# Kernel optimization log

Hardware: AMD Instinct MI355X
Metric: run time of the kernel (lower is better)

The kernel has to match this reference:

```python
import jax, jax.numpy as jnp
import numpy as np
from jax import lax

SD = 16          # sample_duration
STRIDE = 16      # feat_stride
SCALES = (4, 8, 16)
RATIOS = (0.5, 1.0, 2.0)
PRE_NMS = 1000   # proposals kept before NMS (TEST config)
POST_NMS = 128   # proposals kept after NMS
NMS_TH = 0.7


def _anchors2d():
    base = 16.0
    ctr = (base - 1.0) / 2.0
    out = []
    for r in RATIOS:
        ws = np.round(np.sqrt(base * base / r))
        hs = np.round(ws * r)
        for s in SCALES:
            w, h = ws * s, hs * s
            out.append([ctr - (w - 1) / 2, ctr - (h - 1) / 2,
                        ctr + (w - 1) / 2, ctr + (h - 1) / 2])
    return np.asarray(out, np.float32)                       # (9, 4)


def _anchors3d():
    # tube anchors: (x1, y1, t1, x2, y2, t2), durations [SD, SD/2, SD/4]
    a2 = _anchors2d()
    out = []
    for d in (SD, SD // 2, SD // 4):
        for a in a2:
            out.append([a[0], a[1], 0.0, a[2], a[3], d - 1.0])
    return np.asarray(out, np.float32)                       # (27, 6)


def _shifted(anchors, H, W):
    k = anchors.shape[-1]
    sx = jnp.arange(W, dtype=jnp.float32) * STRIDE
    sy = jnp.arange(H, dtype=jnp.float32) * STRIDE
    if k == 4:
        sh = jnp.stack(jnp.broadcast_arrays(sx[None, :], sy[:, None],
                                            sx[None, :], sy[:, None]), -1)
    else:
        z = jnp.zeros((H, W), jnp.float32)
        sh = jnp.stack(jnp.broadcast_arrays(sx[None, :], sy[:, None], z,
                                            sx[None, :], sy[:, None], z), -1)
    return (sh[:, :, None, :] + jnp.asarray(anchors)[None, None]).reshape(-1, k)


def _decode(anchors, deltas):
    # deltas layout: (d_ctr..., d_logsize...); works for 2D (k=4) and 3D (k=6)
    nd = anchors.shape[-1] // 2
    lo, hi = anchors[..., :nd], anchors[..., nd:]
    size = hi - lo + 1.0
    ctr = lo + 0.5 * (size - 1.0)
    pctr = deltas[..., :nd] * size + ctr
    psize = jnp.exp(deltas[..., nd:]) * size
    return jnp.concatenate([pctr - 0.5 * (psize - 1.0),
                            pctr + 0.5 * (psize - 1.0)], -1)


def _iou(b, boxes):
    # b: (k,), boxes: (N, k); area/volume IoU with +1 pixel convention
    nd = boxes.shape[-1] // 2
    lo = jnp.maximum(b[:nd], boxes[:, :nd])
    hi = jnp.minimum(b[nd:], boxes[:, nd:])
    inter = jnp.prod(jnp.maximum(hi - lo + 1.0, 0.0), -1)
    va = jnp.prod(b[nd:] - b[:nd] + 1.0)
    vb = jnp.prod(boxes[:, nd:] - boxes[:, :nd] + 1.0, -1)
    return inter / (va + vb - inter)


def _nms(boxes):
    # boxes already sorted by descending score; greedy NMS, fixed output size
    N = boxes.shape[0]

    def body(i, c):
        supp, keep = c
        idx = jnp.argmax(~supp)                 # first unsuppressed box
        keep = keep.at[i].set(idx.astype(jnp.int32))
        supp = supp | (_iou(boxes[idx], boxes) > NMS_TH)
        supp = supp.at[idx].set(True)
        return supp, keep

    _, keep = lax.fori_loop(0, POST_NMS, body,
                            (jnp.zeros(N, bool), jnp.zeros(POST_NMS, jnp.int32)))
    return keep


def _proposals(scores, deltas, anchors, maxs):
    # scores (B,N), deltas (B,N,k), anchors (N,k), maxs (B,1,k)
    boxes = jnp.clip(_decode(anchors[None], deltas), 0.0, maxs)
    _, idx = lax.top_k(scores, PRE_NMS)
    bx = jnp.take_along_axis(boxes, idx[..., None], axis=1)   # (B,PRE,k)
    keep = jax.vmap(_nms)(bx)                                 # (B,POST)
    sel = jnp.take_along_axis(bx, keep[..., None], axis=1)    # (B,POST,k)
    bidx = jnp.broadcast_to(
        jnp.arange(sel.shape[0], dtype=sel.dtype)[:, None, None],
        sel.shape[:2] + (1,))
    return lax.stop_gradient(jnp.concatenate([bidx, sel], -1))


def setup_inputs() -> dict:
    k = jax.random.split(jax.random.key(0), 8)
    s = 0.01
    return {
        "base_feat": jax.random.normal(k[0], (1, 256, 16, 32, 32), jnp.float32),
        "im_info": jnp.array([[512.0, 512.0, 1.0]], jnp.float32),
        "gt_boxes": jax.random.uniform(k[1], (1, 5, 7), jnp.float32) * 100.0,
        "gt_rois": jax.random.uniform(k[2], (1, 5, 16, 5), jnp.float32) * 100.0,
        "W_conv": jax.random.normal(k[3], (512, 256, 3, 3, 3), jnp.float32) * s,
        "b_conv": jnp.zeros((512,), jnp.float32),
        "W_cls": jax.random.normal(k[4], (54, 512), jnp.float32) * s,
        "b_cls": jnp.zeros((54,), jnp.float32),
        "W_bbox": jax.random.normal(k[5], (162, 512), jnp.float32) * s,
        "b_bbox": jnp.zeros((162,), jnp.float32),
        "W_cls16": jax.random.normal(k[6], (18, 512), jnp.float32) * s,
        "b_cls16": jnp.zeros((18,), jnp.float32),
        "W_bbox16": jax.random.normal(k[7], (36, 512), jnp.float32) * s,
        "b_bbox16": jnp.zeros((36,), jnp.float32),
    }


def reference(base_feat, im_info, gt_boxes, gt_rois, W_conv, b_conv,
              W_cls, b_cls, W_bbox, b_bbox, W_cls16, b_cls16,
              W_bbox16, b_bbox16):
    B, _, T, H, W = base_feat.shape
    # RPN_Conv: 3x3x3 Conv3d + ReLU
    conv1 = jax.nn.relu(
        lax.conv_general_dilated(base_feat, W_conv, (1, 1, 1), "SAME",
                                 dimension_numbers=("NCDHW", "OIDHW", "NCDHW"))
        + b_conv[None, :, None, None, None])
    # 1x1x1 score / bbox heads (3D)
    cls3 = jnp.einsum("bcthw,oc->bothw", conv1, W_cls) + b_cls[None, :, None, None, None]
    bbox3 = jnp.einsum("bcthw,oc->bothw", conv1, W_bbox) + b_bbox[None, :, None, None, None]
    # permute(0,1,3,4,2).mean(4) == mean over the temporal axis
    feat2 = conv1.mean(axis=2)
    cls2 = jnp.einsum("bchw,oc->bohw", feat2, W_cls16) + b_cls16[None, :, None, None]
    bbox2 = jnp.einsum("bchw,oc->bohw", feat2, W_bbox16) + b_bbox16[None, :, None, None]
    # reshape(x,2) + softmax over dim 1; fg prob is the second half of channels
    fg3 = jax.nn.softmax(cls3.reshape(B, 2, 27, T, H, W), axis=1)[:, 1]  # (B,27,T,H,W)
    fg2 = jax.nn.softmax(cls2.reshape(B, 2, 9, H, W), axis=1)[:, 1]      # (B,9,H,W)
    # proposal layers consume detached tensors (torch .data)
    fg3, fg2, bbox3d, bbox2d = map(lax.stop_gradient, (fg3, fg2, bbox3, bbox2))
    # flatten position-major (h, w, anchor)
    sc3 = fg3.mean(axis=2).transpose(0, 2, 3, 1).reshape(B, -1)
    dl3 = bbox3d.mean(axis=2).reshape(B, 27, 6, H, W).transpose(0, 3, 4, 1, 2).reshape(B, -1, 6)
    sc2 = fg2.transpose(0, 2, 3, 1).reshape(B, -1)
    dl2 = bbox2d.reshape(B, 9, 4, H, W).transpose(0, 3, 4, 1, 2).reshape(B, -1, 4)
    imh, imw = im_info[:, 0][:, None], im_info[:, 1][:, None]
    sdm = jnp.full_like(imw, SD - 1.0)
    max3 = jnp.stack([imw - 1, imh - 1, sdm, imw - 1, imh - 1, sdm], -1)  # (B,1,6)
    max2 = jnp.stack([imw - 1, imh - 1, imw - 1, imh - 1], -1)            # (B,1,4)
    rois = _proposals(sc3, dl3, _shifted(_anchors3d(), H, W), max3)       # (B,POST,7)
    rois16 = _proposals(sc2, dl2, _shifted(_anchors2d(), H, W), max2)     # (B,POST,5)
    z = jnp.zeros((), jnp.float32)  # eval mode: all RPN losses are 0
    return rois, rois16, z, z, z, z
```

## Files before the change

### kernel.cpp

```cpp
#include <hip/hip_runtime.h>
#include <hip/hip_bf16.h>
#include <cfloat>
#include <cstdint>


#define T_DIM 16
#define H_DIM 32
#define W_DIM 32
#define NVOX  (T_DIM*H_DIM*W_DIM)
#define HW    (H_DIM*W_DIM)
#define CIN   256
#define COUT  512
#define PRE_NMS 1000
#define POST_NMS 128
#define NMS_TH 0.7f

typedef __attribute__((ext_vector_type(8))) short v8s;
typedef __attribute__((ext_vector_type(4))) float v4f;
typedef __attribute__((ext_vector_type(4))) int v4i;

#define MFMA_B16(A,B,C) __builtin_amdgcn_mfma_f32_16x16x32_bf16(A,B,C,0,0,0)

__device__ __forceinline__ short f2bf(float x) {
    unsigned u = __float_as_uint(x);
    u += 0x7FFFu + ((u >> 16) & 1u);
    return (short)(u >> 16);
}
__device__ __forceinline__ float bf2f(short s) {
    return __uint_as_float(((unsigned)(unsigned short)s) << 16);
}
__device__ __forceinline__ int pk(short a, short b) {
    return (int)((unsigned short)a | ((unsigned)(unsigned short)b << 16));
}

__constant__ float c_ws[3] = {23.f, 16.f, 11.f};
__constant__ float c_hs[3] = {12.f, 16.f, 22.f};
__constant__ float c_sc[3] = {4.f, 8.f, 16.f};
__constant__ float c_depth[3] = {16.f, 8.f, 4.f};

__global__ void k_split_w(const float* __restrict__ W, short* __restrict__ A0,
                          short* __restrict__ A1, short* __restrict__ A2) {
    int i = blockIdx.x * 256 + threadIdx.x;
    int c = i & 255;
    int o = (i >> 8) & 511;
    int tap = i >> 17;
    float x = W[(o * 256 + c) * 27 + tap];
    short h = f2bf(x); float r = x - bf2f(h);
    short m = f2bf(r); float r2 = r - bf2f(m);
    short l = f2bf(r2);
    A0[i] = h; A1[i] = m; A2[i] = l;
}

__global__ void k_build_wcomb(const float* __restrict__ Wcls, const float* __restrict__ Wbb,
                              float* __restrict__ Wc) {
    int i = blockIdx.x * 256 + threadIdx.x;
    int o = i & 255;
    int c = i >> 8;
    float v = 0.f;
    if (o < 54) v = Wcls[o * 512 + c];
    else if (o < 216) v = Wbb[(o - 54) * 512 + c];
    Wc[i] = v;
}


#define SP8(X0,X1,X2,X3,X4,X5,X6,X7, OH, OM, OL) {                            \
    short h0_=f2bf(X0), h1_=f2bf(X1), h2_=f2bf(X2), h3_=f2bf(X3);             \
    short h4_=f2bf(X4), h5_=f2bf(X5), h6_=f2bf(X6), h7_=f2bf(X7);             \
    float r0_=(X0)-bf2f(h0_), r1_=(X1)-bf2f(h1_), r2_=(X2)-bf2f(h2_);         \
    float r3_=(X3)-bf2f(h3_), r4_=(X4)-bf2f(h4_), r5_=(X5)-bf2f(h5_);         \
    float r6_=(X6)-bf2f(h6_), r7_=(X7)-bf2f(h7_);                             \
    short m0_=f2bf(r0_), m1_=f2bf(r1_), m2_=f2bf(r2_), m3_=f2bf(r3_);         \
    short m4_=f2bf(r4_), m5_=f2bf(r5_), m6_=f2bf(r6_), m7_=f2bf(r7_);         \
    short l0_=f2bf(r0_-bf2f(m0_)), l1_=f2bf(r1_-bf2f(m1_));                   \
    short l2_=f2bf(r2_-bf2f(m2_)), l3_=f2bf(r3_-bf2f(m3_));                   \
    short l4_=f2bf(r4_-bf2f(m4_)), l5_=f2bf(r5_-bf2f(m5_));                   \
    short l6_=f2bf(r6_-bf2f(m6_)), l7_=f2bf(r7_-bf2f(m7_));                   \
    OH = (v4i){pk(h0_,h1_), pk(h2_,h3_), pk(h4_,h5_), pk(h6_,h7_)};           \
    OM = (v4i){pk(m0_,m1_), pk(m2_,m3_), pk(m4_,m5_), pk(m6_,m7_)};           \
    OL = (v4i){pk(l0_,l1_), pk(l2_,l3_), pk(l4_,l5_), pk(l6_,l7_)};           \
}

#define CV_SHIFT(TAP) {                                                       \
    int kt_ = (TAP) / 9 - 1, kh_ = ((TAP) / 3) % 3 - 1, kw_ = (TAP) % 3 - 1;  \
    int tt_ = bt + kt_, hh_ = bh + kh_, ww_ = bw + kw_;                       \
    bVal = ((unsigned)tt_ < 16u) && ((unsigned)hh_ < 32u) && ((unsigned)ww_ < 32u); \
    bOff = (tt_ << 10) + (hh_ << 5) + ww_;                                    \
}

#define CV_LOAD_A(TAP, CK) {                                                  \
    size_t ao_ = ((size_t)((TAP) * 512 + o0 + sa_o) << 8) + (CK) + sa_kh * 16;\
    qa00 = *(const v4i*)(A0 + ao_); qa01 = *(const v4i*)(A0 + ao_ + 8);       \
    qa10 = *(const v4i*)(A1 + ao_); qa11 = *(const v4i*)(A1 + ao_ + 8);       \
    qa20 = *(const v4i*)(A2 + ao_); qa21 = *(const v4i*)(A2 + ao_ + 8);       \
}

#define CV_LOAD_B(CK) {                                                       \
    const float* ip_ = I + ((size_t)((CK) + sa_kh * 16) << 14) + bOff;        \
    float x0_  = bVal ? ip_[0]        : 0.f;                                  \
    float x1_  = bVal ? ip_[1 << 14]  : 0.f;                                  \
    float x2_  = bVal ? ip_[2 << 14]  : 0.f;                                  \
    float x3_  = bVal ? ip_[3 << 14]  : 0.f;                                  \
    float x4_  = bVal ? ip_[4 << 14]  : 0.f;                                  \
    float x5_  = bVal ? ip_[5 << 14]  : 0.f;                                  \
    float x6_  = bVal ? ip_[6 << 14]  : 0.f;                                  \
    float x7_  = bVal ? ip_[7 << 14]  : 0.f;                                  \
    float x8_  = bVal ? ip_[8 << 14]  : 0.f;                                  \
    float x9_  = bVal ? ip_[9 << 14]  : 0.f;                                  \
    float x10_ = bVal ? ip_[10 << 14] : 0.f;                                  \
    float x11_ = bVal ? ip_[11 << 14] : 0.f;                                  \
    float x12_ = bVal ? ip_[12 << 14] : 0.f;                                  \
    float x13_ = bVal ? ip_[13 << 14] : 0.f;                                  \
    float x14_ = bVal ? ip_[14 << 14] : 0.f;                                  \
    float x15_ = bVal ? ip_[15 << 14] : 0.f;                                  \
    SP8(x0_,x1_,x2_,x3_,x4_,x5_,x6_,x7_,   pbh0, pbm0, pbl0);                 \
    SP8(x8_,x9_,x10_,x11_,x12_,x13_,x14_,x15_, pbh1, pbm1, pbl1);             \
}

__global__ __launch_bounds__(256) void k_conv3d_mfma(
        const float* __restrict__ I, const short* __restrict__ A0,
        const short* __restrict__ A1, const short* __restrict__ A2,
        const float* __restrict__ bias, float* __restrict__ O) {
    __shared__ __align__(16) short Ash[3][4][128][8];
    __shared__ __align__(16) short Bsh[3][4][128][8];
    const int tid = threadIdx.x;
    const int o0 = blockIdx.y * 128;
    const int v0 = blockIdx.x * 128;
    const int lane = tid & 63, wv = tid >> 6;
    const int quad = lane >> 4, m16 = lane & 15;

    const int sa_o = tid >> 1, sa_kh = tid & 1;
    const int vbase = v0 + sa_o;
    const int bt = vbase >> 10, bh = (vbase >> 5) & 31, bw = vbase & 31;

    v4f acc[2][8];
#pragma unroll
    for (int i = 0; i < 2; i++)
#pragma unroll
        for (int j = 0; j < 8; j++) acc[i][j] = (v4f){0.f, 0.f, 0.f, 0.f};

    int bOff, bVal;
    v4i qa00, qa01, qa10, qa11, qa20, qa21;
    v4i pbh0, pbh1, pbm0, pbm1, pbl0, pbl1;

    CV_SHIFT(0);
    CV_LOAD_A(0, 0);
    CV_LOAD_B(0);

    const int ar0 = wv * 32 + m16;
    const int ar1 = ar0 + 16;

    for (int s = 0; s < 216; ++s) {
        __syncthreads();
        *(v4i*)(&Ash[0][sa_kh * 2    ][sa_o][0]) = qa00;
        *(v4i*)(&Ash[0][sa_kh * 2 + 1][sa_o][0]) = qa01;
        *(v4i*)(&Ash[1][sa_kh * 2    ][sa_o][0]) = qa10;
        *(v4i*)(&Ash[1][sa_kh * 2 + 1][sa_o][0]) = qa11;
        *(v4i*)(&Ash[2][sa_kh * 2    ][sa_o][0]) = qa20;
        *(v4i*)(&Ash[2][sa_kh * 2 + 1][sa_o][0]) = qa21;
        *(v4i*)(&Bsh[0][sa_kh * 2    ][sa_o][0]) = pbh0;
        *(v4i*)(&Bsh[0][sa_kh * 2 + 1][sa_o][0]) = pbh1;
        *(v4i*)(&Bsh[1][sa_kh * 2    ][sa_o][0]) = pbm0;
        *(v4i*)(&Bsh[1][sa_kh * 2 + 1][sa_o][0]) = pbm1;
        *(v4i*)(&Bsh[2][sa_kh * 2    ][sa_o][0]) = pbl0;
        *(v4i*)(&Bsh[2][sa_kh * 2 + 1][sa_o][0]) = pbl1;
        __syncthreads();
        {
            int s1 = s + 1;
            if (s1 < 216) {
                int tap1 = s1 >> 3, ck1 = (s1 & 7) << 5;
                if ((s1 & 7) == 0) CV_SHIFT(tap1);
                CV_LOAD_A(tap1, ck1);
                CV_LOAD_B(ck1);
            }
        }
        v8s ah0 = *(const v8s*)(&Ash[0][quad][ar0][0]);
        v8s ah1 = *(const v8s*)(&Ash[0][quad][ar1][0]);
        v8s am0 = *(const v8s*)(&Ash[1][quad][ar0][0]);
        v8s am1 = *(const v8s*)(&Ash[1][quad][ar1][0]);
        v8s al0 = *(const v8s*)(&Ash[2][quad][ar0][0]);
        v8s al1 = *(const v8s*)(&Ash[2][quad][ar1][0]);
#pragma unroll
        for (int vt = 0; vt < 8; ++vt) {
            int vr = vt * 16 + m16;
            v8s bb = *(const v8s*)(&Bsh[0][quad][vr][0]);
            v8s bm = *(const v8s*)(&Bsh[1][quad][vr][0]);
            v8s bl = *(const v8s*)(&Bsh[2][quad][vr][0]);
            v4f a0 = acc[0][vt];
            a0 = MFMA_B16(ah0, bb, a0);
            a0 = MFMA_B16(ah0, bm, a0);
            a0 = MFMA_B16(am0, bb, a0);
            a0 = MFMA_B16(ah0, bl, a0);
            a0 = MFMA_B16(am0, bm, a0);
            a0 = MFMA_B16(al0, bb, a0);
            acc[0][vt] = a0;
            v4f a1 = acc[1][vt];
            a1 = MFMA_B16(ah1, bb, a1);
            a1 = MFMA_B16(ah1, bm, a1);
            a1 = MFMA_B16(am1, bb, a1);
            a1 = MFMA_B16(ah1, bl, a1);
            a1 = MFMA_B16(am1, bm, a1);
            a1 = MFMA_B16(al1, bb, a1);
            acc[1][vt] = a1;
        }
    }

#pragma unroll
    for (int ot = 0; ot < 2; ++ot) {
#pragma unroll
        for (int r = 0; r < 4; ++r) {
            int o = o0 + wv * 32 + ot * 16 + quad * 4 + r;
            float bo = bias[o];
            float* dst = O + (size_t)o * NVOX + v0 + m16;
#pragma unroll
            for (int vt = 0; vt < 8; ++vt)
                dst[vt * 16] = fmaxf(acc[ot][vt][r] + bo, 0.f);
        }
    }
}

__global__ __launch_bounds__(256) void k_gemm_logits3(const float* __restrict__ conv1,
                                                      const float* __restrict__ Wc,
                                                      float* __restrict__ L) {
    __shared__ float As[16][128];
    __shared__ float Bs[16][128];
    const int tid = threadIdx.x;
    const int o0 = blockIdx.y * 128;
    const int v0 = blockIdx.x * 128;
    const int ty = tid >> 4, tx = tid & 15;

    float acc[8][8];
#pragma unroll
    for (int i = 0; i < 8; i++)
#pragma unroll
        for (int j = 0; j < 8; j++) acc[i][j] = 0.f;

    for (int ck = 0; ck < 512; ck += 16) {
        __syncthreads();
#pragma unroll
        for (int r = 0; r < 2; ++r) {
            int f = tid + r * 256;
            int c_l = f >> 5, o4 = (f & 31) << 2;
            *(float4*)(&As[c_l][o4]) = *(const float4*)(Wc + ((size_t)(ck + c_l) << 8) + o0 + o4);
        }
#pragma unroll
        for (int r = 0; r < 2; ++r) {
            int f = tid + r * 256;
            int c_l = f >> 5, v4 = (f & 31) << 2;
            *(float4*)(&Bs[c_l][v4]) = *(const float4*)(conv1 + ((size_t)(ck + c_l) << 14) + v0 + v4);
        }
        __syncthreads();
#pragma unroll
        for (int k = 0; k < 16; ++k) {
            float a[8], b[8];
            *(float4*)(a)     = *(const float4*)(&As[k][ty * 4]);
            *(float4*)(a + 4) = *(const float4*)(&As[k][64 + ty * 4]);
            *(float4*)(b)     = *(const float4*)(&Bs[k][tx * 4]);
            *(float4*)(b + 4) = *(const float4*)(&Bs[k][64 + tx * 4]);
#pragma unroll
            for (int i = 0; i < 8; i++)
#pragma unroll
                for (int j = 0; j < 8; j++)
                    acc[i][j] = fmaf(a[i], b[j], acc[i][j]);
        }
    }
#pragma unroll
    for (int i = 0; i < 8; i++) {
        int orow = (i < 4) ? (ty * 4 + i) : (64 + ty * 4 + (i - 4));
        float* dst = L + (size_t)(o0 + orow) * NVOX + v0;
        *(float4*)(dst + tx * 4)      = *(const float4*)(&acc[i][0]);
        *(float4*)(dst + 64 + tx * 4) = *(const float4*)(&acc[i][4]);
    }
}

__global__ void k_sc3(const float* __restrict__ L, const float* __restrict__ b_cls,
                      float* __restrict__ sc3) {
    int i = blockIdx.x * 256 + threadIdx.x;
    if (i >= 27 * HW) return;
    int a = i >> 10, hw = i & 1023;
    float b0 = b_cls[a], b1 = b_cls[27 + a];
    const float* L0 = L + (size_t)a * NVOX + hw;
    const float* L1 = L + (size_t)(27 + a) * NVOX + hw;
    float s = 0.f;
    for (int t = 0; t < T_DIM; t++) {
        float x0 = L0[t * HW] + b0, x1 = L1[t * HW] + b1;
        float m = fmaxf(x0, x1);
        float e0 = expf(x0 - m), e1 = expf(x1 - m);
        s += e1 / (e0 + e1);
    }
    sc3[hw * 27 + a] = s * (1.f / 16.f);
}

__global__ void k_dl3(const float* __restrict__ L, const float* __restrict__ b_bbox,
                      float* __restrict__ dl3) {
    int i = blockIdx.x * 256 + threadIdx.x;
    if (i >= 162 * HW) return;
    int ch = i >> 10, hw = i & 1023;
    const float* Lr = L + (size_t)(54 + ch) * NVOX + hw;
    float s = 0.f;
    for (int t = 0; t < T_DIM; t++) s += Lr[t * HW];
    s = s * (1.f / 16.f) + b_bbox[ch];
    int a = ch / 6, d = ch - a * 6;
    dl3[((size_t)hw * 27 + a) * 6 + d] = s;
}

__global__ void k_feat2(const float* __restrict__ conv1, float* __restrict__ feat2) {
    int i = blockIdx.x * 256 + threadIdx.x;
    int c = i >> 10, hw = i & 1023;
    const float* src = conv1 + (size_t)c * NVOX + hw;
    float s = 0.f;
    for (int t = 0; t < T_DIM; t++) s += src[t * HW];
    feat2[i] = s * (1.f / 16.f);
}

__global__ void k_gemm2d(const float* __restrict__ feat2, const float* __restrict__ Wcls16,
                         const float* __restrict__ Wbb16, float* __restrict__ L2) {
    int g = blockIdx.x * 256 + threadIdx.x;
    int o = g >> 10, hw = g & 1023;
    const float* wrow = (o < 18) ? (Wcls16 + (size_t)o * 512) : (Wbb16 + (size_t)(o - 18) * 512);
    float s = 0.f;
    for (int c = 0; c < 512; c++) s = fmaf(wrow[c], feat2[(size_t)c * HW + hw], s);
    L2[(size_t)o * HW + hw] = s;
}

__global__ void k_sc2(const float* __restrict__ L2, const float* __restrict__ b_cls16,
                      float* __restrict__ sc2) {
    int i = blockIdx.x * 256 + threadIdx.x;
    if (i >= 9 * HW) return;
    int a = i >> 10, hw = i & 1023;
    float x0 = L2[(size_t)a * HW + hw] + b_cls16[a];
    float x1 = L2[(size_t)(9 + a) * HW + hw] + b_cls16[9 + a];
    float m = fmaxf(x0, x1);
    float e0 = expf(x0 - m), e1 = expf(x1 - m);
    sc2[hw * 9 + a] = e1 / (e0 + e1);
}

__global__ void k_dl2(const float* __restrict__ L2, const float* __restrict__ b_bbox16,
                      float* __restrict__ dl2) {
    int i = blockIdx.x * 256 + threadIdx.x;
    if (i >= 36 * HW) return;
    int ch = i >> 10, hw = i & 1023;
    float v = L2[(size_t)(18 + ch) * HW + hw] + b_bbox16[ch];
    int a = ch >> 2, d = ch & 3;
    dl2[((size_t)hw * 9 + a) * 4 + d] = v;
}

__device__ __forceinline__ unsigned mapf(float f) {
    unsigned u = __float_as_uint(f);
    return (u & 0x80000000u) ? ~u : (u | 0x80000000u);
}

__global__ __launch_bounds__(1024) void k_proposal(const float* __restrict__ im_info,
                                                   const float* __restrict__ sc3,
                                                   const float* __restrict__ dl3,
                                                   const float* __restrict__ sc2,
                                                   const float* __restrict__ dl2,
                                                   float* __restrict__ out) {
    const int branch = blockIdx.x;
    const int tid = threadIdx.x;
    const int A = (branch == 0) ? 27 : 9;
    const int nd = (branch == 0) ? 3 : 2;
    const float* scores = (branch == 0) ? sc3 : sc2;
    const float* deltas = (branch == 0) ? dl3 : dl2;
    const int K = PRE_NMS;
    const int ept = A;
    const int base = tid * ept;

    __shared__ unsigned hist[256];
    __shared__ unsigned long long keys[1024];
    __shared__ float bx[PRE_NMS][6];
    __shared__ int keep[POST_NMS];
    __shared__ unsigned wsum[16];
    __shared__ unsigned long long alive[16];
    __shared__ int sh_b, sh_next, bcast;

    unsigned prefix = 0;
    int rank = K;
    for (int shift = 24; shift >= 0; shift -= 8) {
        if (tid < 256) hist[tid] = 0;
        __syncthreads();
        const unsigned mask_hi = (shift == 24) ? 0u : (0xFFFFFFFFu << (shift + 8));
        for (int j = 0; j < ept; j++) {
            unsigned m = mapf(scores[base + j]);
            if ((m & mask_hi) == prefix)
                atomicAdd(&hist[(m >> shift) & 255], 1u);
        }
        __syncthreads();
        for (int d = 1; d < 256; d <<= 1) {
            unsigned add = 0;
            if (tid < 256 && tid + d < 256) add = hist[tid + d];
            __syncthreads();
            if (tid < 256) hist[tid] += add;
            __syncthreads();
        }
        if (tid < 256) {
            bool win = (hist[tid] >= (unsigned)rank) &&
                       (tid == 255 || hist[tid + 1] < (unsigned)rank);
            if (win) { sh_b = tid; sh_next = (tid == 255) ? 0 : (int)hist[tid + 1]; }
        }
        __syncthreads();
        prefix |= (unsigned)sh_b << shift;
        rank -= sh_next;
        __syncthreads();
    }
    const unsigned tau = prefix;

    int gt_c = 0, eq_c = 0;
    for (int j = 0; j < ept; j++) {
        unsigned m = mapf(scores[base + j]);
        gt_c += (m > tau);
        eq_c += (m == tau);
    }
    unsigned cnt = ((unsigned)gt_c << 16) | (unsigned)eq_c;
    const int lane = tid & 63, wid = tid >> 6;
    unsigned x = cnt;
    for (int d = 1; d < 64; d <<= 1) {
        unsigned y = __shfl_up(x, d);
        if (lane >= d) x += y;
    }
    if (lane == 63) wsum[wid] = x;
    __syncthreads();
    if (wid == 0) {
        unsigned w = (lane < 16) ? wsum[lane] : 0;
        for (int d = 1; d < 16; d <<= 1) {
            unsigned y = __shfl_up(w, d);
            if (lane >= d) w += y;
        }
        if (lane < 16) wsum[lane] = w;
    }
    __syncthreads();
    unsigned excl = x - cnt + (wid ? wsum[wid - 1] : 0);
    const int c1 = (int)(wsum[15] >> 16);
    int gi = (int)(excl >> 16);
    int ei = (int)(excl & 0xFFFFu);
    for (int j = 0; j < ept; j++) {
        int idx = base + j;
        unsigned m = mapf(scores[idx]);
        unsigned long long key = ((unsigned long long)m << 32) |
                                 (unsigned)(0xFFFFFFFFu - (unsigned)idx);
        if (m > tau) {
            keys[gi++] = key;
        } else if (m == tau) {
            if (c1 + ei < K) keys[c1 + ei] = key;
            ei++;
        }
    }
    if (tid < 1024 - K) keys[K + tid] = 0;
    __syncthreads();

    for (int k = 2; k <= 1024; k <<= 1) {
        for (int j = k >> 1; j > 0; j >>= 1) {
            int ixj = tid ^ j;
            if (ixj > tid) {
                unsigned long long a = keys[tid], b = keys[ixj];
                bool sw = ((tid & k) == 0) ? (a < b) : (a > b);
                if (sw) { keys[tid] = b; keys[ixj] = a; }
            }
            __syncthreads();
        }
    }

    const float imh = im_info[0], imw = im_info[1];
    if (tid < K) {
        int n = (int)(0xFFFFFFFFu - (unsigned)(keys[tid] & 0xFFFFFFFFull));
        int cell = n / A, a = n - cell * A;
        int hc = cell >> 5, wc = cell & 31;
        int a2 = (branch == 0) ? (a % 9) : a;
        int ri = a2 / 3, si = a2 % 3;
        float w = c_ws[ri] * c_sc[si], h = c_hs[ri] * c_sc[si];
        float lo[3], hi[3], mx[3];
        lo[0] = 7.5f - (w - 1.f) * 0.5f + 16.f * wc;
        hi[0] = 7.5f + (w - 1.f) * 0.5f + 16.f * wc;
        mx[0] = imw - 1.f;
        lo[1] = 7.5f - (h - 1.f) * 0.5f + 16.f * hc;
        hi[1] = 7.5f + (h - 1.f) * 0.5f + 16.f * hc;
        mx[1] = imh - 1.f;
        if (branch == 0) { lo[2] = 0.f; hi[2] = c_depth[a / 9] - 1.f; mx[2] = (float)(T_DIM - 1); }
        const float* dp = deltas + (size_t)n * (2 * nd);
        for (int d = 0; d < nd; d++) {
            float size = hi[d] - lo[d] + 1.f;
            float ctr = lo[d] + 0.5f * (size - 1.f);
            float pctr = dp[d] * size + ctr;
            float psize = expf(dp[nd + d]) * size;
            float pl = pctr - 0.5f * (psize - 1.f);
            float ph = pctr + 0.5f * (psize - 1.f);
            bx[tid][d]      = fminf(fmaxf(pl, 0.f), mx[d]);
            bx[tid][nd + d] = fminf(fmaxf(ph, 0.f), mx[d]);
        }
    }
    if (tid < 16) alive[tid] = (tid < 15) ? ~0ull : ((1ull << (K - 15 * 64)) - 1);
    __syncthreads();

    float myb[6]; float myvol = 1.f;
    if (tid < K) {
        for (int d = 0; d < 6; d++) myb[d] = bx[tid][d];
        for (int d = 0; d < nd; d++) myvol *= (myb[nd + d] - myb[d] + 1.f);
    }
    for (int i = 0; i < POST_NMS; ++i) {
        if (tid < 64) {
            unsigned long long wv = (tid < 16) ? alive[tid] : 0ull;
            int cand = wv ? (tid * 64 + __ffsll(wv) - 1) : 0x7fffffff;
#pragma unroll
            for (int off = 32; off; off >>= 1)
                cand = min(cand, __shfl_xor(cand, off));
            if (tid == 0) {
                int m = (cand == 0x7fffffff) ? 0 : cand;
                bcast = m; keep[i] = m;
            }
        }
        __syncthreads();
        int sel = bcast;
        bool s = false;
        if (tid < K) {
            float inter = 1.f, selvol = 1.f;
            for (int d = 0; d < nd; d++) {
                float slo = bx[sel][d], shi = bx[sel][nd + d];
                float l = fmaxf(slo, myb[d]);
                float hh = fminf(shi, myb[nd + d]);
                inter *= fmaxf(hh - l + 1.f, 0.f);
                selvol *= (shi - slo + 1.f);
            }
            float iou = inter / (selvol + myvol - inter);
            s = (iou > NMS_TH) || (tid == sel);
        }
        unsigned long long bal = __ballot(s);
        if (lane == 0 && bal) alive[wid] &= ~bal;
        __syncthreads();
    }

    if (tid < POST_NMS) {
        int k = keep[tid];
        if (branch == 0) {
            float* o = out + (size_t)tid * 7;
            o[0] = 0.f;
            for (int d = 0; d < 6; d++) o[1 + d] = bx[k][d];
        } else {
            float* o = out + 128 * 7 + (size_t)tid * 5;
            o[0] = 0.f;
            for (int d = 0; d < 4; d++) o[1 + d] = bx[k][d];
        }
    }
    if (branch == 0 && tid == 0) {
        out[1536] = 0.f; out[1537] = 0.f; out[1538] = 0.f; out[1539] = 0.f;
    }
}

extern "C" void kernel_launch(void* const* d_in, const int* in_sizes, int n_in,
                              void* d_out, int out_size, void* d_ws, size_t ws_size,
                              hipStream_t stream) {
    (void)in_sizes; (void)n_in; (void)out_size; (void)ws_size;
    const float* base_feat = (const float*)d_in[0];
    const float* im_info   = (const float*)d_in[1];
    const float* W_conv    = (const float*)d_in[4];
    const float* b_conv    = (const float*)d_in[5];
    const float* W_cls     = (const float*)d_in[6];
    const float* b_cls     = (const float*)d_in[7];
    const float* W_bbox    = (const float*)d_in[8];
    const float* b_bbox    = (const float*)d_in[9];
    const float* W_cls16   = (const float*)d_in[10];
    const float* b_cls16   = (const float*)d_in[11];
    const float* W_bbox16  = (const float*)d_in[12];
    const float* b_bbox16  = (const float*)d_in[13];
    float* out = (float*)d_out;

    char* ws = (char*)d_ws;
    const size_t AW = (size_t)27 * 512 * 256;
    short* A0 = (short*)ws;
    short* A1 = A0 + AW;
    short* A2 = A1 + AW;
    float* L3 = (float*)ws;
    size_t off = AW * 3 * sizeof(short);
    float* Wcomb  = (float*)(ws + off); off += (size_t)512 * 256 * 4;
    float* conv1  = (float*)(ws + off); off += (size_t)COUT * NVOX * 4;
    float* feat2  = (float*)(ws + off); off += (size_t)512 * HW * 4;
    float* L2     = (float*)(ws + off); off += (size_t)64 * HW * 4;
    float* sc3    = (float*)(ws + off); off += (size_t)27 * HW * 4;
    float* dl3    = (float*)(ws + off); off += (size_t)27 * HW * 6 * 4;
    float* sc2    = (float*)(ws + off); off += (size_t)9 * HW * 4;
    float* dl2    = (float*)(ws + off); off += (size_t)9 * HW * 4 * 4;

    k_split_w<<<13824, 256, 0, stream>>>(W_conv, A0, A1, A2);
    k_build_wcomb<<<512, 256, 0, stream>>>(W_cls, W_bbox, Wcomb);
    {
        dim3 g(NVOX / 128, COUT / 128);
        k_conv3d_mfma<<<g, 256, 0, stream>>>(base_feat, A0, A1, A2, b_conv, conv1);
    }
    {
        dim3 g(NVOX / 128, 2);
        k_gemm_logits3<<<g, 256, 0, stream>>>(conv1, Wcomb, L3);
    }
    k_sc3<<<(27 * HW + 255) / 256, 256, 0, stream>>>(L3, b_cls, sc3);
    k_dl3<<<(162 * HW + 255) / 256, 256, 0, stream>>>(L3, b_bbox, dl3);
    k_feat2<<<(512 * HW) / 256, 256, 0, stream>>>(conv1, feat2);
    k_gemm2d<<<(54 * HW) / 256, 256, 0, stream>>>(feat2, W_cls16, W_bbox16, L2);
    k_sc2<<<(9 * HW + 255) / 256, 256, 0, stream>>>(L2, b_cls16, sc2);
    k_dl2<<<(36 * HW + 255) / 256, 256, 0, stream>>>(L2, b_bbox16, dl2);
    k_proposal<<<2, 1024, 0, stream>>>(im_info, sc3, dl3, sc2, dl2, out);
}
```

Measured before the change: 1.119 ms.

## Retile conv3d MFMA warps to 64x64 and swizzle LDS layout

The conv3d MFMA kernel now gives each wave a 64x64 output tile in a 2x2 arrangement instead of 32x128. This cuts the LDS fragment reads per MFMA, since each wave loads 4 A and 4 B fragment groups rather than 2 A and 8 B. The shared-memory staging is flattened to v4i arrays with an XOR swizzle on the k-chunk index, meant to avoid bank conflicts on stores and reads. Out-of-bounds input offsets are also clamped to zero. The rest is variable renaming with no speed intent.

```diff
diff --git a/kernel.cpp b/kernel.cpp
--- a/kernel.cpp
+++ b/kernel.cpp
@@ -61,7 +61,6 @@
     else if (o < 216) v = Wbb[(o - 54) * 512 + c];
     Wc[i] = v;
 }
-
 
 #define SP8(X0,X1,X2,X3,X4,X5,X6,X7, OH, OM, OL) {                            \
     short h0_=f2bf(X0), h1_=f2bf(X1), h2_=f2bf(X2), h3_=f2bf(X3);             \
@@ -84,18 +83,18 @@
     int kt_ = (TAP) / 9 - 1, kh_ = ((TAP) / 3) % 3 - 1, kw_ = (TAP) % 3 - 1;  \
     int tt_ = bt + kt_, hh_ = bh + kh_, ww_ = bw + kw_;                       \
     bVal = ((unsigned)tt_ < 16u) && ((unsigned)hh_ < 32u) && ((unsigned)ww_ < 32u); \
-    bOff = (tt_ << 10) + (hh_ << 5) + ww_;                                    \
+    bOff = bVal ? ((tt_ << 10) + (hh_ << 5) + ww_) : 0;                       \
 }
 
 #define CV_LOAD_A(TAP, CK) {                                                  \
-    size_t ao_ = ((size_t)((TAP) * 512 + o0 + sa_o) << 8) + (CK) + sa_kh * 16;\
-    qa00 = *(const v4i*)(A0 + ao_); qa01 = *(const v4i*)(A0 + ao_ + 8);       \
-    qa10 = *(const v4i*)(A1 + ao_); qa11 = *(const v4i*)(A1 + ao_ + 8);       \
-    qa20 = *(const v4i*)(A2 + ao_); qa21 = *(const v4i*)(A2 + ao_ + 8);       \
+    size_t ao_ = ((size_t)((TAP) * 512 + o0 + sr) << 8) + (CK) + skh * 16;    \
+    pa0 = *(const v4i*)(A0 + ao_); pa1 = *(const v4i*)(A0 + ao_ + 8);         \
+    pa2 = *(const v4i*)(A1 + ao_); pa3 = *(const v4i*)(A1 + ao_ + 8);         \
+    pa4 = *(const v4i*)(A2 + ao_); pa5 = *(const v4i*)(A2 + ao_ + 8);         \
 }
 
 #define CV_LOAD_B(CK) {                                                       \
-    const float* ip_ = I + ((size_t)((CK) + sa_kh * 16) << 14) + bOff;        \
+    const float* ip_ = I + ((size_t)((CK) + skh * 16) << 14) + bOff;          \
     float x0_  = bVal ? ip_[0]        : 0.f;                                  \
     float x1_  = bVal ? ip_[1 << 14]  : 0.f;                                  \
     float x2_  = bVal ? ip_[2 << 14]  : 0.f;                                  \
@@ -112,7 +111,7 @@
     float x13_ = bVal ? ip_[13 << 14] : 0.f;                                  \
     float x14_ = bVal ? ip_[14 << 14] : 0.f;                                  \
     float x15_ = bVal ? ip_[15 << 14] : 0.f;                                  \
-    SP8(x0_,x1_,x2_,x3_,x4_,x5_,x6_,x7_,   pbh0, pbm0, pbl0);                 \
+    SP8(x0_,x1_,x2_,x3_,x4_,x5_,x6_,x7_,       pbh0, pbm0, pbl0);             \
     SP8(x8_,x9_,x10_,x11_,x12_,x13_,x14_,x15_, pbh1, pbm1, pbl1);             \
 }
 
@@ -120,49 +119,51 @@
         const float* __restrict__ I, const short* __restrict__ A0,
         const short* __restrict__ A1, const short* __restrict__ A2,
         const float* __restrict__ bias, float* __restrict__ O) {
-    __shared__ __align__(16) short Ash[3][4][128][8];
-    __shared__ __align__(16) short Bsh[3][4][128][8];
+    __shared__ v4i Ash[3][512];
+    __shared__ v4i Bsh[3][512];
     const int tid = threadIdx.x;
     const int o0 = blockIdx.y * 128;
     const int v0 = blockIdx.x * 128;
-    const int lane = tid & 63, wv = tid >> 6;
+    const int lane = tid & 63;
+    const int wv = tid >> 6;
     const int quad = lane >> 4, m16 = lane & 15;
-
-    const int sa_o = tid >> 1, sa_kh = tid & 1;
-    const int vbase = v0 + sa_o;
+    const int wo = (wv >> 1) * 64;
+    const int wvx = (wv & 1) * 64;
+
+    const int sr = ((tid >> 6) & 1) * 64 + (tid & 63);
+    const int skh = tid >> 7;
+    const int uW0 = sr * 4 + ((skh * 2) ^ ((sr >> 2) & 3));
+    const int uW1 = sr * 4 + ((skh * 2 + 1) ^ ((sr >> 2) & 3));
+
+    const int vbase = v0 + sr;
     const int bt = vbase >> 10, bh = (vbase >> 5) & 31, bw = vbase & 31;
 
-    v4f acc[2][8];
-#pragma unroll
-    for (int i = 0; i < 2; i++)
-#pragma unroll
-        for (int j = 0; j < 8; j++) acc[i][j] = (v4f){0.f, 0.f, 0.f, 0.f};
+    const int sw = quad ^ (m16 >> 2);
+    const int uA = (wo + m16) * 4 + sw;
+    const int uB = (wvx + m16) * 4 + sw;
+
+    v4f acc[4][4];
+#pragma unroll
+    for (int i = 0; i < 4; i++)
+#pragma unroll
+        for (int j = 0; j < 4; j++) acc[i][j] = (v4f){0.f, 0.f, 0.f, 0.f};
 
     int bOff, bVal;
-    v4i qa00, qa01, qa10, qa11, qa20, qa21;
+    v4i pa0, pa1, pa2, pa3, pa4, pa5;
     v4i pbh0, pbh1, pbm0, pbm1, pbl0, pbl1;
 
     CV_SHIFT(0);
     CV_LOAD_A(0, 0);
     CV_LOAD_B(0);
 
-    const int ar0 = wv * 32 + m16;
-    const int ar1 = ar0 + 16;
-
     for (int s = 0; s < 216; ++s) {
         __syncthreads();
-        *(v4i*)(&Ash[0][sa_kh * 2    ][sa_o][0]) = qa00;
-        *(v4i*)(&Ash[0][sa_kh * 2 + 1][sa_o][0]) = qa01;
-        *(v4i*)(&Ash[1][sa_kh * 2    ][sa_o][0]) = qa10;
-        *(v4i*)(&Ash[1][sa_kh * 2 + 1][sa_o][0]) = qa11;
-        *(v4i*)(&Ash[2][sa_kh * 2    ][sa_o][0]) = qa20;
-        *(v4i*)(&Ash[2][sa_kh * 2 + 1][sa_o][0]) = qa21;
-        *(v4i*)(&Bsh[0][sa_kh * 2    ][sa_o][0]) = pbh0;
-        *(v4i*)(&Bsh[0][sa_kh * 2 + 1][sa_o][0]) = pbh1;
-        *(v4i*)(&Bsh[1][sa_kh * 2    ][sa_o][0]) = pbm0;
-        *(v4i*)(&Bsh[1][sa_kh * 2 + 1][sa_o][0]) = pbm1;
-        *(v4i*)(&Bsh[2][sa_kh * 2    ][sa_o][0]) = pbl0;
-        *(v4i*)(&Bsh[2][sa_kh * 2 + 1][sa_o][0]) = pbl1;
+        Ash[0][uW0] = pa0; Ash[0][uW1] = pa1;
+        Ash[1][uW0] = pa2; Ash[1][uW1] = pa3;
+        Ash[2][uW0] = pa4; Ash[2][uW1] = pa5;
+        Bsh[0][uW0] = pbh0; Bsh[0][uW1] = pbh1;
+        Bsh[1][uW0] = pbm0; Bsh[1][uW1] = pbm1;
+        Bsh[2][uW0] = pbl0; Bsh[2][uW1] = pbl1;
         __syncthreads();
         {
             int s1 = s + 1;
@@ -173,47 +174,57 @@
                 CV_LOAD_B(ck1);
             }
         }
-        v8s ah0 = *(const v8s*)(&Ash[0][quad][ar0][0]);
-        v8s ah1 = *(const v8s*)(&Ash[0][quad][ar1][0]);
-        v8s am0 = *(const v8s*)(&Ash[1][quad][ar0][0]);
-        v8s am1 = *(const v8s*)(&Ash[1][quad][ar1][0]);
-        v8s al0 = *(const v8s*)(&Ash[2][quad][ar0][0]);
-        v8s al1 = *(const v8s*)(&Ash[2][quad][ar1][0]);
-#pragma unroll
-        for (int vt = 0; vt < 8; ++vt) {
-            int vr = vt * 16 + m16;
-            v8s bb = *(const v8s*)(&Bsh[0][quad][vr][0]);
-            v8s bm = *(const v8s*)(&Bsh[1][quad][vr][0]);
-            v8s bl = *(const v8s*)(&Bsh[2][quad][vr][0]);
-            v4f a0 = acc[0][vt];
-            a0 = MFMA_B16(ah0, bb, a0);
-            a0 = MFMA_B16(ah0, bm, a0);
-            a0 = MFMA_B16(am0, bb, a0);
-            a0 = MFMA_B16(ah0, bl, a0);
-            a0 = MFMA_B16(am0, bm, a0);
-            a0 = MFMA_B16(al0, bb, a0);
-            acc[0][vt] = a0;
-            v4f a1 = acc[1][vt];
-            a1 = MFMA_B16(ah1, bb, a1);
-            a1 = MFMA_B16(ah1, bm, a1);
-            a1 = MFMA_B16(am1, bb, a1);
-            a1 = MFMA_B16(ah1, bl, a1);
-            a1 = MFMA_B16(am1, bm, a1);
-            a1 = MFMA_B16(al1, bb, a1);
-            acc[1][vt] = a1;
-        }
-    }
-
-#pragma unroll
-    for (int ot = 0; ot < 2; ++ot) {
+        v8s ah0 = *(const v8s*)(&Ash[0][uA]);
+        v8s ah1 = *(const v8s*)(&Ash[0][uA + 64]);
+        v8s ah2 = *(const v8s*)(&Ash[0][uA + 128]);
+        v8s ah3 = *(const v8s*)(&Ash[0][uA + 192]);
+        v8s am0 = *(const v8s*)(&Ash[1][uA]);
+        v8s am1 = *(const v8s*)(&Ash[1][uA + 64]);
+        v8s am2 = *(const v8s*)(&Ash[1][uA + 128]);
+        v8s am3 = *(const v8s*)(&Ash[1][uA + 192]);
+        v8s al0 = *(const v8s*)(&Ash[2][uA]);
+        v8s al1 = *(const v8s*)(&Ash[2][uA + 64]);
+        v8s al2 = *(const v8s*)(&Ash[2][uA + 128]);
+        v8s al3 = *(const v8s*)(&Ash[2][uA + 192]);
+#pragma unroll
+        for (int j = 0; j < 4; ++j) {
+            v8s bb = *(const v8s*)(&Bsh[0][uB + j * 64]);
+            v8s bm = *(const v8s*)(&Bsh[1][uB + j * 64]);
+            v8s bl = *(const v8s*)(&Bsh[2][uB + j * 64]);
+            v4f a;
+            a = acc[0][j];
+            a = MFMA_B16(ah0, bb, a); a = MFMA_B16(ah0, bm, a);
+            a = MFMA_B16(am0, bb, a); a = MFMA_B16(ah0, bl, a);
+            a = MFMA_B16(am0, bm, a); a = MFMA_B16(al0, bb, a);
+            acc[0][j] = a;
+            a = acc[1][j];
+            a = MFMA_B16(ah1, bb, a); a = MFMA_B16(ah1, bm, a);
+            a = MFMA_B16(am1, bb, a); a = MFMA_B16(ah1, bl, a);
+            a = MFMA_B16(am1, bm, a); a = MFMA_B16(al1, bb, a);
+            acc[1][j] = a;
+            a = acc[2][j];
+            a = MFMA_B16(ah2, bb, a); a = MFMA_B16(ah2, bm, a);
+            a = MFMA_B16(am2, bb, a); a = MFMA_B16(ah2, bl, a);
+            a = MFMA_B16(am2, bm, a); a = MFMA_B16(al2, bb, a);
+            acc[2][j] = a;
+            a = acc[3][j];
+            a = MFMA_B16(ah3, bb, a); a = MFMA_B16(ah3, bm, a);
+            a = MFMA_B16(am3, bb, a); a = MFMA_B16(ah3, bl, a);
+            a = MFMA_B16(am3, bm, a); a = MFMA_B16(al3, bb, a);
+            acc[3][j] = a;
+        }
+    }
+
+#pragma unroll
+    for (int i = 0; i < 4; ++i) {
 #pragma unroll
         for (int r = 0; r < 4; ++r) {
-            int o = o0 + wv * 32 + ot * 16 + quad * 4 + r;
+            int o = o0 + wo + i * 16 + quad * 4 + r;
             float bo = bias[o];
-            float* dst = O + (size_t)o * NVOX + v0 + m16;
-#pragma unroll
-            for (int vt = 0; vt < 8; ++vt)
-                dst[vt * 16] = fmaxf(acc[ot][vt][r] + bo, 0.f);
+            float* dst = O + (size_t)o * NVOX + v0 + wvx + m16;
+#pragma unroll
+            for (int j = 0; j < 4; ++j)
+                dst[j * 16] = fmaxf(acc[i][j][r] + bo, 0.f);
         }
     }
 }
@@ -452,8 +463,8 @@
             int ixj = tid ^ j;
             if (ixj > tid) {
                 unsigned long long a = keys[tid], b = keys[ixj];
-                bool sw = ((tid & k) == 0) ? (a < b) : (a > b);
-                if (sw) { keys[tid] = b; keys[ixj] = a; }
+                bool sw2 = ((tid & k) == 0) ? (a < b) : (a > b);
+                if (sw2) { keys[tid] = b; keys[ixj] = a; }
             }
             __syncthreads();
         }
@@ -497,8 +508,8 @@
     }
     for (int i = 0; i < POST_NMS; ++i) {
         if (tid < 64) {
-            unsigned long long wv = (tid < 16) ? alive[tid] : 0ull;
-            int cand = wv ? (tid * 64 + __ffsll(wv) - 1) : 0x7fffffff;
+            unsigned long long wvb = (tid < 16) ? alive[tid] : 0ull;
+            int cand = wvb ? (tid * 64 + __ffsll(wvb) - 1) : 0x7fffffff;
 #pragma unroll
             for (int off = 32; off; off >>= 1)
                 cand = min(cand, __shfl_xor(cand, off));
```

Measured after the change: 1.143 ms. +2.2%, slower.
